# Kernel optimization log

Measured on AMD Instinct MI355X. Metric: run time of the kernel, lower is better.

The kernel has to match this reference:

```python
import jax, jax.numpy as jnp
import numpy as np

BN_EPS = 1e-5
NEG_SLOPE = 0.2

def _avgpool2(x):
    B, C, H, W = x.shape
    return x.reshape(B, C, H // 2, 2, W // 2, 2).mean(axis=(3, 5))

def _conv1x1(x, w, b):
    # x: [B,C,H,W], w: [O,C], b: [O]
    return jnp.einsum('bchw,oc->bohw', x, w) + b[None, :, None, None]

def _bilinear_resize(x, out_h, out_w):
    # PyTorch F.interpolate(mode='bilinear', align_corners=False) semantics
    B, C, h, w = x.shape
    ys = jnp.maximum((jnp.arange(out_h, dtype=jnp.float32) + 0.5) * (h / out_h) - 0.5, 0.0)
    xs = jnp.maximum((jnp.arange(out_w, dtype=jnp.float32) + 0.5) * (w / out_w) - 0.5, 0.0)
    y0 = jnp.floor(ys).astype(jnp.int32); x0 = jnp.floor(xs).astype(jnp.int32)
    wy = (ys - y0.astype(jnp.float32)).astype(x.dtype)
    wx = (xs - x0.astype(jnp.float32)).astype(x.dtype)
    y1 = jnp.minimum(y0 + 1, h - 1); x1 = jnp.minimum(x0 + 1, w - 1)
    rows = x[:, :, y0, :] * (1.0 - wy)[None, None, :, None] + x[:, :, y1, :] * wy[None, None, :, None]
    out = rows[:, :, :, x0] * (1.0 - wx)[None, None, None, :] + rows[:, :, :, x1] * wx[None, None, None, :]
    return out

def setup_inputs() -> dict:
    key = jax.random.key(0)
    ks = jax.random.split(key, 16)
    B, Cin, Hid, Cout, H, W = 8, 64, 64, 64, 128, 128
    s = 0.05
    return {
        'rgb': jax.random.normal(ks[0], (B, Cin, H, W), dtype=jnp.float32),
        'freq': jax.random.normal(ks[1], (B, Cin, H, W), dtype=jnp.float32),
        'w_q': jax.random.normal(ks[2], (Hid, Cin), dtype=jnp.float32) * s,
        'b_q': jax.random.normal(ks[3], (Hid,), dtype=jnp.float32) * s,
        'w_k': jax.random.normal(ks[4], (Hid, Cin), dtype=jnp.float32) * s,
        'b_k': jax.random.normal(ks[5], (Hid,), dtype=jnp.float32) * s,
        'w_v': jax.random.normal(ks[6], (Hid, Cin), dtype=jnp.float32) * s,
        'b_v': jax.random.normal(ks[7], (Hid,), dtype=jnp.float32) * s,
        'w_o': jax.random.normal(ks[8], (Cout, Hid), dtype=jnp.float32) * s,
        'b_o': jax.random.normal(ks[9], (Cout,), dtype=jnp.float32) * s,
        'bn_gamma': jnp.ones((Cout,), dtype=jnp.float32),
        'bn_beta': jnp.zeros((Cout,), dtype=jnp.float32),
        'bn_mean': jax.random.normal(ks[10], (Cout,), dtype=jnp.float32) * s,
        'bn_var': jax.random.uniform(ks[11], (Cout,), dtype=jnp.float32, minval=0.5, maxval=1.5),
    }

def reference(rgb, freq, w_q, b_q, w_k, b_k, w_v, b_v, w_o, b_o, bn_gamma, bn_beta, bn_mean, bn_var):
    B, C, H, W = rgb.shape
    rgb_ds = _avgpool2(rgb)
    freq_ds = _avgpool2(freq)
    hd, wd = rgb_ds.shape[2], rgb_ds.shape[3]
    hid = w_q.shape[0]
    scale = hid ** (-0.5)
    # 1x1 conv QKV projections, flatten spatial dims to tokens N = hd*wd
    q = _conv1x1(rgb_ds, w_q, b_q).reshape(B, hid, hd * wd)   # [B,hid,N]
    k = _conv1x1(freq_ds, w_k, b_k).reshape(B, hid, hd * wd)  # [B,hid,N]
    v = _conv1x1(freq_ds, w_v, b_v).reshape(B, hid, hd * wd)  # [B,hid,N]
    attn = jax.nn.softmax(jnp.einsum('bcn,bcm->bnm', q, k) * scale, axis=-1)  # [B,N,N]
    z = jnp.einsum('bnm,bcm->bcn', attn, v).reshape(B, hid, hd, wd)
    z = _bilinear_resize(z, H, W)
    y = _conv1x1(z, w_o, b_o)
    # inference-mode BatchNorm fused as affine
    inv = bn_gamma / jnp.sqrt(bn_var + BN_EPS)
    y = (y - bn_mean[None, :, None, None]) * inv[None, :, None, None] + bn_beta[None, :, None, None]
    y = jnp.where(y >= 0, y, NEG_SLOPE * y)  # LeakyReLU(0.2)
    return rgb + y
```

## Files before the change

### kernel.cpp

```cpp
#include <hip/hip_runtime.h>
#include <hip/hip_bf16.h>

typedef unsigned short u16;
typedef unsigned int   u32;
typedef __attribute__((ext_vector_type(8))) short bf16x8;
typedef __attribute__((ext_vector_type(4))) float f32x4;

__device__ __forceinline__ u16 f2bf(float f) {
  u32 u = __float_as_uint(f);
  u32 r = u + 0x7fffu + ((u >> 16) & 1u);
  return (u16)(r >> 16);
}
__device__ __forceinline__ float bflo(u32 u) { return __uint_as_float(u << 16); }
__device__ __forceinline__ float bfhi(u32 u) { return __uint_as_float(u & 0xffff0000u); }
__device__ __forceinline__ u32 packhi(float a, float b) {
  return __builtin_amdgcn_perm(__float_as_uint(b), __float_as_uint(a), 0x07060302u);
}

__global__ __launch_bounds__(256, 4) void k_qkv(
    const float* __restrict__ rgb, const float* __restrict__ freq,
    const float* __restrict__ wq, const float* __restrict__ bq,
    const float* __restrict__ wk, const float* __restrict__ bk,
    const float* __restrict__ wv, const float* __restrict__ bv,
    u16* __restrict__ Qo, u16* __restrict__ Ko, u16* __restrict__ Vo)
{
  __shared__ __align__(16) u16 sm[3 * 4608];
  u16* X  = sm;
  u16* W0 = sm + 4608;
  u16* W1 = sm + 9216;

  const int t    = threadIdx.x;
  const int side = blockIdx.x & 1;
  const int seg  = blockIdx.x >> 1;
  const int idx0 = seg * 64;
  const int bb   = idx0 >> 12;
  const int n0   = idx0 & 4095;
  const int h    = n0 >> 6;
  const float* src = side ? freq : rgb;

  const size_t sbase = (size_t)bb * 64 * 16384 + (size_t)(2 * h) * 128;
  {
    const int tokp = t & 31;
    const int grp  = t >> 5;
    const float* p0 = src + sbase + 4 * tokp + (size_t)(grp * 8) * 16384;
    u32 pk0[4], pk1[4];
#pragma unroll
    for (int c = 0; c < 8; c += 2) {
      const float* pa = p0 + (size_t)c * 16384;
      float4 a0 = *(const float4*)pa;
      float4 a1 = *(const float4*)(pa + 128);
      float t0a = 0.25f * ((a0.x + a0.y) + (a1.x + a1.y));
      float t1a = 0.25f * ((a0.z + a0.w) + (a1.z + a1.w));
      const float* pb = pa + 16384;
      float4 c0 = *(const float4*)pb;
      float4 c1 = *(const float4*)(pb + 128);
      float t0b = 0.25f * ((c0.x + c0.y) + (c1.x + c1.y));
      float t1b = 0.25f * ((c0.z + c0.w) + (c1.z + c1.w));
      pk0[c >> 1] = (u32)f2bf(t0a) | ((u32)f2bf(t0b) << 16);
      pk1[c >> 1] = (u32)f2bf(t1a) | ((u32)f2bf(t1b) << 16);
    }
    uint4 qv0; qv0.x = pk0[0]; qv0.y = pk0[1]; qv0.z = pk0[2]; qv0.w = pk0[3];
    uint4 qv1; qv1.x = pk1[0]; qv1.y = pk1[1]; qv1.z = pk1[2]; qv1.w = pk1[3];
    *(uint4*)&X[(2 * tokp) * 72 + grp * 8] = qv0;
    *(uint4*)&X[(2 * tokp + 1) * 72 + grp * 8] = qv1;
  }
  {
    const int o = t >> 2, c0 = (t & 3) << 4;
    const float4* p4 = (const float4*)((side ? wk : wq) + o * 64 + c0);
    float4 f0 = p4[0], f1 = p4[1], f2 = p4[2], f3 = p4[3];
    uint4 qa, qb;
    qa.x = (u32)f2bf(f0.x) | ((u32)f2bf(f0.y) << 16);
    qa.y = (u32)f2bf(f0.z) | ((u32)f2bf(f0.w) << 16);
    qa.z = (u32)f2bf(f1.x) | ((u32)f2bf(f1.y) << 16);
    qa.w = (u32)f2bf(f1.z) | ((u32)f2bf(f1.w) << 16);
    qb.x = (u32)f2bf(f2.x) | ((u32)f2bf(f2.y) << 16);
    qb.y = (u32)f2bf(f2.z) | ((u32)f2bf(f2.w) << 16);
    qb.z = (u32)f2bf(f3.x) | ((u32)f2bf(f3.y) << 16);
    qb.w = (u32)f2bf(f3.z) | ((u32)f2bf(f3.w) << 16);
    *(uint4*)&W0[o * 72 + c0] = qa;
    *(uint4*)&W0[o * 72 + c0 + 8] = qb;
    if (side) {
      const float4* v4 = (const float4*)(wv + o * 64 + c0);
      float4 g0 = v4[0], g1 = v4[1], g2 = v4[2], g3 = v4[3];
      qa.x = (u32)f2bf(g0.x) | ((u32)f2bf(g0.y) << 16);
      qa.y = (u32)f2bf(g0.z) | ((u32)f2bf(g0.w) << 16);
      qa.z = (u32)f2bf(g1.x) | ((u32)f2bf(g1.y) << 16);
      qa.w = (u32)f2bf(g1.z) | ((u32)f2bf(g1.w) << 16);
      qb.x = (u32)f2bf(g2.x) | ((u32)f2bf(g2.y) << 16);
      qb.y = (u32)f2bf(g2.z) | ((u32)f2bf(g2.w) << 16);
      qb.z = (u32)f2bf(g3.x) | ((u32)f2bf(g3.y) << 16);
      qb.w = (u32)f2bf(g3.z) | ((u32)f2bf(g3.w) << 16);
      *(uint4*)&W1[o * 72 + c0] = qa;
      *(uint4*)&W1[o * 72 + c0 + 8] = qb;
    }
  }
  __syncthreads();

  const int lane = t & 63, w = t >> 6;
  const int l15 = lane & 15, qd = lane >> 4;
  const int tb = w * 16;

  bf16x8 af0 = *(const bf16x8*)&X[(tb + l15) * 72 + qd * 8];
  bf16x8 af1 = *(const bf16x8*)&X[(tb + l15) * 72 + 32 + qd * 8];

  f32x4 acc[4];
#pragma unroll
  for (int nt = 0; nt < 4; ++nt) {
    bf16x8 b0 = *(const bf16x8*)&W0[(nt * 16 + l15) * 72 + qd * 8];
    bf16x8 b1 = *(const bf16x8*)&W0[(nt * 16 + l15) * 72 + 32 + qd * 8];
    f32x4 a = {0.f, 0.f, 0.f, 0.f};
    a = __builtin_amdgcn_mfma_f32_16x16x32_bf16(af0, b0, a, 0, 0, 0);
    a = __builtin_amdgcn_mfma_f32_16x16x32_bf16(af1, b1, a, 0, 0, 0);
    acc[nt] = a;
  }
  {
    const float* bias0 = side ? bk : bq;
    const float sc = side ? 1.f : 0.18033688f;
    u16* dst0 = side ? Ko : Qo;
#pragma unroll
    for (int nt = 0; nt < 4; ++nt) {
      float bia = bias0[nt * 16 + l15];
#pragma unroll
      for (int e = 0; e < 4; ++e) {
        int tok = idx0 + tb + qd * 4 + e;
        dst0[(size_t)tok * 64 + nt * 16 + l15] = f2bf((acc[nt][e] + bia) * sc);
      }
    }
  }

  if (side) {
    f32x4 accv[4];
#pragma unroll
    for (int ct = 0; ct < 4; ++ct) {
      bf16x8 a0 = *(const bf16x8*)&W1[(ct * 16 + l15) * 72 + qd * 8];
      bf16x8 a1 = *(const bf16x8*)&W1[(ct * 16 + l15) * 72 + 32 + qd * 8];
      f32x4 a = {0.f, 0.f, 0.f, 0.f};
      a = __builtin_amdgcn_mfma_f32_16x16x32_bf16(a0, af0, a, 0, 0, 0);
      a = __builtin_amdgcn_mfma_f32_16x16x32_bf16(a1, af1, a, 0, 0, 0);
      accv[ct] = a;
    }
#pragma unroll
    for (int ct = 0; ct < 4; ++ct) {
#pragma unroll
      for (int e = 0; e < 4; ++e) {
        int c = ct * 16 + qd * 4 + e;
        float v = accv[ct][e] + bv[c];
        Vo[((size_t)(bb * 64 + c)) * 4096 + n0 + tb + l15] = f2bf(v);
      }
    }
  }
}

__global__ __launch_bounds__(256, 2) void k_attn(
    const u16* __restrict__ Qg, const u16* __restrict__ Kg,
    const u16* __restrict__ Vg,
    const float* __restrict__ wo, const float* __restrict__ bo,
    const float* __restrict__ gam, const float* __restrict__ bet,
    const float* __restrict__ mean, const float* __restrict__ var,
    u16* __restrict__ Ya)
{
  __shared__ __align__(16) u16 Pb[4 * 4608];
  __shared__ __align__(16) u16 Wl[4608];
  __shared__ __align__(16) u16 Zc[4608];
  __shared__ float lb[256];
  __shared__ float Afs[64], Bfs[64];

  const int b  = blockIdx.x;
  const int q0 = blockIdx.y * 64;
  const int t  = threadIdx.x;
  const int lane = t & 63, w = t >> 6;
  const int l15 = lane & 15, qd = lane >> 4;
  u16* P = Pb + w * 4608;

  {
    const int o = t >> 2, c0 = (t & 3) << 4;
    const float4* p4 = (const float4*)(wo + o * 64 + c0);
    float4 f0 = p4[0], f1 = p4[1], f2 = p4[2], f3 = p4[3];
    uint4 qa, qb;
    qa.x = (u32)f2bf(f0.x) | ((u32)f2bf(f0.y) << 16);
    qa.y = (u32)f2bf(f0.z) | ((u32)f2bf(f0.w) << 16);
    qa.z = (u32)f2bf(f1.x) | ((u32)f2bf(f1.y) << 16);
    qa.w = (u32)f2bf(f1.z) | ((u32)f2bf(f1.w) << 16);
    qb.x = (u32)f2bf(f2.x) | ((u32)f2bf(f2.y) << 16);
    qb.y = (u32)f2bf(f2.z) | ((u32)f2bf(f2.w) << 16);
    qb.z = (u32)f2bf(f3.x) | ((u32)f2bf(f3.y) << 16);
    qb.w = (u32)f2bf(f3.z) | ((u32)f2bf(f3.w) << 16);
    *(uint4*)&Wl[o * 72 + c0] = qa;
    *(uint4*)&Wl[o * 72 + c0 + 8] = qb;
    if (t < 64) {
      float A = gam[t] * __frsqrt_rn(var[t] + 1e-5f);
      Afs[t] = A;
      Bfs[t] = (bo[t] - mean[t]) * A + bet[t];
    }
  }

  bf16x8 qf[4][2];
#pragma unroll
  for (int qt = 0; qt < 4; ++qt) {
    const u16* p = Qg + ((size_t)(b * 4096 + q0 + qt * 16 + l15)) * 64 + qd * 8;
    qf[qt][0] = *(const bf16x8*)p;
    qf[qt][1] = *(const bf16x8*)(p + 32);
  }

  f32x4 zacc[4][4];
#pragma unroll
  for (int i = 0; i < 4; ++i)
#pragma unroll
    for (int j = 0; j < 4; ++j) {
      f32x4 z = {0.f, 0.f, 0.f, 0.f};
      zacc[i][j] = z;
    }
  float lacc[4] = {0.f, 0.f, 0.f, 0.f};

  for (int tile = 0; tile < 16; ++tile) {
    const int n0 = w * 1024 + tile * 64;

    bf16x8 kf[4][2], vf[4][2];
#pragma unroll
    for (int mt = 0; mt < 4; ++mt) {
      const u16* p = Kg + ((size_t)(b * 4096 + n0 + mt * 16 + l15)) * 64 + qd * 8;
      kf[mt][0] = *(const bf16x8*)p;
      kf[mt][1] = *(const bf16x8*)(p + 32);
    }
#pragma unroll
    for (int ct = 0; ct < 4; ++ct) {
      const u16* p = Vg + ((size_t)(b * 64 + ct * 16 + l15)) * 4096 + n0 + qd * 8;
      vf[ct][0] = *(const bf16x8*)p;
      vf[ct][1] = *(const bf16x8*)(p + 32);
    }

#pragma unroll
    for (int qt = 0; qt < 4; ++qt) {
#pragma unroll
      for (int mt = 0; mt < 4; ++mt) {
        f32x4 a = {0.f, 0.f, 0.f, 0.f};
        __builtin_amdgcn_s_setprio(1);
        a = __builtin_amdgcn_mfma_f32_16x16x32_bf16(kf[mt][0], qf[qt][0], a, 0, 0, 0);
        a = __builtin_amdgcn_mfma_f32_16x16x32_bf16(kf[mt][1], qf[qt][1], a, 0, 0, 0);
        __builtin_amdgcn_s_setprio(0);
        float p0 = __builtin_amdgcn_exp2f(a[0]);
        float p1 = __builtin_amdgcn_exp2f(a[1]);
        float p2 = __builtin_amdgcn_exp2f(a[2]);
        float p3 = __builtin_amdgcn_exp2f(a[3]);
        lacc[qt] += (p0 + p1) + (p2 + p3);
        uint2 pw;
        pw.x = packhi(p0, p1);
        pw.y = packhi(p2, p3);
        *(uint2*)&P[(qt * 16 + l15) * 72 + mt * 16 + qd * 4] = pw;
      }
    }
#pragma unroll
    for (int qt = 0; qt < 4; ++qt) {
      bf16x8 pf0 = *(const bf16x8*)&P[(qt * 16 + l15) * 72 + qd * 8];
      bf16x8 pf1 = *(const bf16x8*)&P[(qt * 16 + l15) * 72 + 32 + qd * 8];
      __builtin_amdgcn_s_setprio(1);
#pragma unroll
      for (int ct = 0; ct < 4; ++ct) {
        zacc[ct][qt] = __builtin_amdgcn_mfma_f32_16x16x32_bf16(vf[ct][0], pf0, zacc[ct][qt], 0, 0, 0);
        zacc[ct][qt] = __builtin_amdgcn_mfma_f32_16x16x32_bf16(vf[ct][1], pf1, zacc[ct][qt], 0, 0, 0);
      }
      __builtin_amdgcn_s_setprio(0);
    }
  }

#pragma unroll
  for (int qt = 0; qt < 4; ++qt) {
    float l = lacc[qt];
    l += __shfl_xor(l, 16);
    l += __shfl_xor(l, 32);
    lb[w * 64 + qt * 16 + l15] = l;
  }
#pragma unroll
  for (int qt = 0; qt < 4; ++qt)
#pragma unroll
    for (int ct = 0; ct < 4; ++ct) {
      uint2 pw;
      pw.x = packhi(zacc[ct][qt][0], zacc[ct][qt][1]);
      pw.y = packhi(zacc[ct][qt][2], zacc[ct][qt][3]);
      *(uint2*)&P[(qt * 16 + l15) * 72 + ct * 16 + qd * 4] = pw;
    }
  __syncthreads();

  {
    const u32* Pu = (const u32*)Pb;
    u32* Zu = (u32*)Zc;
#pragma unroll
    for (int i = 0; i < 8; ++i) {
      int cell = i * 256 + t;
      int q = cell >> 5, cu = cell & 31;
      float s0 = 0.f, s1 = 0.f;
#pragma unroll
      for (int ww = 0; ww < 4; ++ww) {
        u32 v = Pu[ww * 2304 + q * 36 + cu];
        s0 += bflo(v);
        s1 += bfhi(v);
      }
      float inv = 1.f / (lb[q] + lb[64 + q] + lb[128 + q] + lb[192 + q]);
      Zu[q * 36 + cu] = packhi(s0 * inv, s1 * inv);
    }
  }
  __syncthreads();

  {
    bf16x8 af0 = *(const bf16x8*)&Zc[(w * 16 + l15) * 72 + qd * 8];
    bf16x8 af1 = *(const bf16x8*)&Zc[(w * 16 + l15) * 72 + 32 + qd * 8];
#pragma unroll
    for (int nt = 0; nt < 4; ++nt) {
      bf16x8 b0 = *(const bf16x8*)&Wl[(nt * 16 + l15) * 72 + qd * 8];
      bf16x8 b1 = *(const bf16x8*)&Wl[(nt * 16 + l15) * 72 + 32 + qd * 8];
      f32x4 y = {0.f, 0.f, 0.f, 0.f};
      y = __builtin_amdgcn_mfma_f32_16x16x32_bf16(b0, af0, y, 0, 0, 0);
      y = __builtin_amdgcn_mfma_f32_16x16x32_bf16(b1, af1, y, 0, 0, 0);
#pragma unroll
      for (int e = 0; e < 4; ++e) {
        const int o = nt * 16 + qd * 4 + e;
        float v = y[e] * Afs[o] + Bfs[o];
        Ya[((size_t)(b * 64 + o)) * 4096 + q0 + w * 16 + l15] =
            (u16)(__float_as_uint(v) >> 16);
      }
    }
  }
}

__global__ __launch_bounds__(256, 8) void k_out(
    const u16* __restrict__ Ya, const float* __restrict__ rgb,
    float* __restrict__ out)
{
  const int tid = blockIdx.x * 256 + threadIdx.x;
  const int g = tid & 31;
  const int i = (tid >> 5) & 127;
  const int o = (tid >> 12) & 63;
  const int b = tid >> 18;

  float ys = fmaxf(0.5f * (float)i - 0.25f, 0.f);
  int   y0 = (int)ys;
  float wy = ys - (float)y0;
  int   y1 = min(y0 + 1, 63);

  const u32* Yw = (const u32*)(Ya + ((size_t)(b * 64 + o)) * 4096);
  const int base0 = y0 * 32, base1 = y1 * 32;
  const int gm = (g == 0) ? 0 : g - 1;
  const int gp = (g == 31) ? 31 : g + 1;

  u32 tm = Yw[base0 + gm], t0 = Yw[base0 + g], tp = Yw[base0 + gp];
  u32 bm = Yw[base1 + gm], b0w = Yw[base1 + g], bp = Yw[base1 + gp];

  const float iw = 1.f - wy;
  float r_m1 = iw * bfhi(tm) + wy * bfhi(bm);
  float r_0  = iw * bflo(t0) + wy * bflo(b0w);
  float r_1  = iw * bfhi(t0) + wy * bfhi(b0w);
  float r_2  = iw * bflo(tp) + wy * bflo(bp);

  float v0 = (g == 0)  ? r_0 : 0.25f * r_m1 + 0.75f * r_0;
  float v1 = 0.75f * r_0 + 0.25f * r_1;
  float v2 = 0.25f * r_0 + 0.75f * r_1;
  float v3 = (g == 31) ? r_1 : 0.75f * r_1 + 0.25f * r_2;

  v0 = (v0 >= 0.f) ? v0 : 0.2f * v0;
  v1 = (v1 >= 0.f) ? v1 : 0.2f * v1;
  v2 = (v2 >= 0.f) ? v2 : 0.2f * v2;
  v3 = (v3 >= 0.f) ? v3 : 0.2f * v3;

  const size_t pix = ((size_t)((b * 64 + o) * 128 + i)) * 128 + g * 4;
  float4 rv = *(const float4*)(rgb + pix);
  float4 ov;
  ov.x = rv.x + v0;
  ov.y = rv.y + v1;
  ov.z = rv.z + v2;
  ov.w = rv.w + v3;
  *(float4*)(out + pix) = ov;
}

extern "C" void kernel_launch(void* const* d_in, const int* in_sizes, int n_in,
                              void* d_out, int out_size, void* d_ws, size_t ws_size,
                              hipStream_t stream) {
  (void)in_sizes; (void)n_in; (void)out_size; (void)ws_size;
  const float* rgb  = (const float*)d_in[0];
  const float* freq = (const float*)d_in[1];
  const float* wq   = (const float*)d_in[2];
  const float* bq   = (const float*)d_in[3];
  const float* wk   = (const float*)d_in[4];
  const float* bk   = (const float*)d_in[5];
  const float* wv   = (const float*)d_in[6];
  const float* bv   = (const float*)d_in[7];
  const float* wo   = (const float*)d_in[8];
  const float* bo   = (const float*)d_in[9];
  const float* gam  = (const float*)d_in[10];
  const float* bet  = (const float*)d_in[11];
  const float* mean = (const float*)d_in[12];
  const float* var  = (const float*)d_in[13];

  char* ws = (char*)d_ws;
  u16* Qw = (u16*)(ws);
  u16* Kw = (u16*)(ws + 4194304);
  u16* Vw = (u16*)(ws + 8388608);
  u16* Yw = (u16*)(ws + 12582912);

  k_qkv<<<dim3(1024), dim3(256), 0, stream>>>(rgb, freq, wq, bq, wk, bk, wv, bv,
                                              Qw, Kw, Vw);
  k_attn<<<dim3(8, 64), dim3(256), 0, stream>>>(Qw, Kw, Vw, wo, bo, gam, bet,
                                                mean, var, Yw);
  k_out<<<dim3(8192), dim3(256), 0, stream>>>(Yw, rgb, (float*)d_out);
}
```

Before: 201.3 us.

## Double-buffer K/V register loads in attention loop and coalesce Y stores via LDS

The attention inner loop is unrolled by two with ping-pong K fragment registers. The next tile's K and V global loads are issued before the current tile's MFMA work, with sched barriers to keep that order, so memory latency overlaps compute. The epilogue now stages the projected output in shared memory and writes it with 16-byte coalesced stores instead of scattered 2-byte stores. This raises register pressure, which could reduce occupancy or cause spills, and adds one extra barrier.

Result: slower. 261.5 us (+29.9%).

```diff
diff --git a/kernel.cpp b/kernel.cpp
--- a/kernel.cpp
+++ b/kernel.cpp
@@ -212,56 +212,78 @@
     }
   float lacc[4] = {0.f, 0.f, 0.f, 0.f};
 
-  for (int tile = 0; tile < 16; ++tile) {
-    const int n0 = w * 1024 + tile * 64;
-
-    bf16x8 kf[4][2], vf[4][2];
-#pragma unroll
-    for (int mt = 0; mt < 4; ++mt) {
-      const u16* p = Kg + ((size_t)(b * 4096 + n0 + mt * 16 + l15)) * 64 + qd * 8;
-      kf[mt][0] = *(const bf16x8*)p;
-      kf[mt][1] = *(const bf16x8*)(p + 32);
-    }
-#pragma unroll
-    for (int ct = 0; ct < 4; ++ct) {
-      const u16* p = Vg + ((size_t)(b * 64 + ct * 16 + l15)) * 4096 + n0 + qd * 8;
-      vf[ct][0] = *(const bf16x8*)p;
-      vf[ct][1] = *(const bf16x8*)(p + 32);
-    }
-
-#pragma unroll
-    for (int qt = 0; qt < 4; ++qt) {
-#pragma unroll
-      for (int mt = 0; mt < 4; ++mt) {
-        f32x4 a = {0.f, 0.f, 0.f, 0.f};
-        __builtin_amdgcn_s_setprio(1);
-        a = __builtin_amdgcn_mfma_f32_16x16x32_bf16(kf[mt][0], qf[qt][0], a, 0, 0, 0);
-        a = __builtin_amdgcn_mfma_f32_16x16x32_bf16(kf[mt][1], qf[qt][1], a, 0, 0, 0);
-        __builtin_amdgcn_s_setprio(0);
-        float p0 = __builtin_amdgcn_exp2f(a[0]);
-        float p1 = __builtin_amdgcn_exp2f(a[1]);
-        float p2 = __builtin_amdgcn_exp2f(a[2]);
-        float p3 = __builtin_amdgcn_exp2f(a[3]);
-        lacc[qt] += (p0 + p1) + (p2 + p3);
-        uint2 pw;
-        pw.x = packhi(p0, p1);
-        pw.y = packhi(p2, p3);
-        *(uint2*)&P[(qt * 16 + l15) * 72 + mt * 16 + qd * 4] = pw;
-      }
-    }
-#pragma unroll
-    for (int qt = 0; qt < 4; ++qt) {
-      bf16x8 pf0 = *(const bf16x8*)&P[(qt * 16 + l15) * 72 + qd * 8];
-      bf16x8 pf1 = *(const bf16x8*)&P[(qt * 16 + l15) * 72 + 32 + qd * 8];
-      __builtin_amdgcn_s_setprio(1);
-#pragma unroll
-      for (int ct = 0; ct < 4; ++ct) {
-        zacc[ct][qt] = __builtin_amdgcn_mfma_f32_16x16x32_bf16(vf[ct][0], pf0, zacc[ct][qt], 0, 0, 0);
-        zacc[ct][qt] = __builtin_amdgcn_mfma_f32_16x16x32_bf16(vf[ct][1], pf1, zacc[ct][qt], 0, 0, 0);
-      }
-      __builtin_amdgcn_s_setprio(0);
-    }
-  }
+#define LOADK(DST, P_) do {                                                   \
+    DST[0][0] = *(const bf16x8*)(P_);          DST[0][1] = *(const bf16x8*)((P_) + 32);   \
+    DST[1][0] = *(const bf16x8*)((P_) + 1024); DST[1][1] = *(const bf16x8*)((P_) + 1056); \
+    DST[2][0] = *(const bf16x8*)((P_) + 2048); DST[2][1] = *(const bf16x8*)((P_) + 2080); \
+    DST[3][0] = *(const bf16x8*)((P_) + 3072); DST[3][1] = *(const bf16x8*)((P_) + 3104); \
+  } while (0)
+#define LOADV(DST, P_) do {                                                   \
+    DST[0][0] = *(const bf16x8*)(P_);            DST[0][1] = *(const bf16x8*)((P_) + 32);     \
+    DST[1][0] = *(const bf16x8*)((P_) + 65536);  DST[1][1] = *(const bf16x8*)((P_) + 65568);  \
+    DST[2][0] = *(const bf16x8*)((P_) + 131072); DST[2][1] = *(const bf16x8*)((P_) + 131104); \
+    DST[3][0] = *(const bf16x8*)((P_) + 196608); DST[3][1] = *(const bf16x8*)((P_) + 196640); \
+  } while (0)
+#define QK_PHASE(KF) do {                                                     \
+    _Pragma("unroll")                                                         \
+    for (int qt = 0; qt < 4; ++qt) {                                          \
+      _Pragma("unroll")                                                       \
+      for (int mt = 0; mt < 4; ++mt) {                                        \
+        f32x4 a = {0.f, 0.f, 0.f, 0.f};                                       \
+        __builtin_amdgcn_s_setprio(1);                                        \
+        a = __builtin_amdgcn_mfma_f32_16x16x32_bf16(KF[mt][0], qf[qt][0], a, 0, 0, 0); \
+        a = __builtin_amdgcn_mfma_f32_16x16x32_bf16(KF[mt][1], qf[qt][1], a, 0, 0, 0); \
+        __builtin_amdgcn_s_setprio(0);                                        \
+        float p0 = __builtin_amdgcn_exp2f(a[0]);                              \
+        float p1 = __builtin_amdgcn_exp2f(a[1]);                              \
+        float p2 = __builtin_amdgcn_exp2f(a[2]);                              \
+        float p3 = __builtin_amdgcn_exp2f(a[3]);                              \
+        lacc[qt] += (p0 + p1) + (p2 + p3);                                    \
+        uint2 pw;                                                             \
+        pw.x = packhi(p0, p1);                                                \
+        pw.y = packhi(p2, p3);                                                \
+        *(uint2*)&P[(qt * 16 + l15) * 72 + mt * 16 + qd * 4] = pw;            \
+      }                                                                       \
+    }                                                                         \
+  } while (0)
+#define PV_PHASE(VF) do {                                                     \
+    _Pragma("unroll")                                                         \
+    for (int qt = 0; qt < 4; ++qt) {                                          \
+      bf16x8 pf0 = *(const bf16x8*)&P[(qt * 16 + l15) * 72 + qd * 8];         \
+      bf16x8 pf1 = *(const bf16x8*)&P[(qt * 16 + l15) * 72 + 32 + qd * 8];    \
+      __builtin_amdgcn_s_setprio(1);                                          \
+      _Pragma("unroll")                                                       \
+      for (int ct = 0; ct < 4; ++ct) {                                        \
+        zacc[ct][qt] = __builtin_amdgcn_mfma_f32_16x16x32_bf16(VF[ct][0], pf0, zacc[ct][qt], 0, 0, 0); \
+        zacc[ct][qt] = __builtin_amdgcn_mfma_f32_16x16x32_bf16(VF[ct][1], pf1, zacc[ct][qt], 0, 0, 0); \
+      }                                                                       \
+      __builtin_amdgcn_s_setprio(0);                                          \
+    }                                                                         \
+  } while (0)
+
+  const u16* kp = Kg + ((size_t)(b * 4096 + w * 1024 + l15)) * 64 + qd * 8;
+  const u16* vp = Vg + ((size_t)(b * 64 + l15)) * 4096 + w * 1024 + qd * 8;
+  bf16x8 kfA[4][2], kfB[4][2], vf[4][2];
+
+  LOADK(kfA, kp); kp += 4096;
+  for (int it = 0; it < 8; ++it) {
+    LOADV(vf, vp); vp += 64;
+    QK_PHASE(kfA);
+    LOADK(kfB, kp); kp += 4096;
+    __builtin_amdgcn_sched_barrier(0);
+    PV_PHASE(vf);
+    LOADV(vf, vp); vp += 64;
+    QK_PHASE(kfB);
+    if (it < 7) {
+      LOADK(kfA, kp); kp += 4096;
+      __builtin_amdgcn_sched_barrier(0);
+    }
+    PV_PHASE(vf);
+  }
+#undef LOADK
+#undef LOADV
+#undef QK_PHASE
+#undef PV_PHASE
 
 #pragma unroll
   for (int qt = 0; qt < 4; ++qt) {
@@ -302,6 +324,7 @@
   __syncthreads();
 
   {
+    u16* Ys = Pb;
     bf16x8 af0 = *(const bf16x8*)&Zc[(w * 16 + l15) * 72 + qd * 8];
     bf16x8 af1 = *(const bf16x8*)&Zc[(w * 16 + l15) * 72 + 32 + qd * 8];
 #pragma unroll
@@ -315,10 +338,18 @@
       for (int e = 0; e < 4; ++e) {
         const int o = nt * 16 + qd * 4 + e;
         float v = y[e] * Afs[o] + Bfs[o];
-        Ya[((size_t)(b * 64 + o)) * 4096 + q0 + w * 16 + l15] =
-            (u16)(__float_as_uint(v) >> 16);
+        Ys[o * 72 + w * 16 + l15] = (u16)(__float_as_uint(v) >> 16);
       }
     }
+  }
+  __syncthreads();
+  {
+    const int o = t >> 2, c4 = (t & 3) << 4;
+    uint4 y0 = *(const uint4*)&Pb[o * 72 + c4];
+    uint4 y1 = *(const uint4*)&Pb[o * 72 + c4 + 8];
+    u16* d = Ya + ((size_t)(b * 64 + o)) * 4096 + q0;
+    *(uint4*)&d[c4] = y0;
+    *(uint4*)&d[c4 + 8] = y1;
   }
 }
 
```
